# Performance work log

Hardware: AMD Instinct MI355X
Metric: run time of the kernel (lower is better)

Reference implementation:

```python
import jax, jax.numpy as jnp
import numpy as np

EMB_DIM = 1024
NUM_HEADS = 16
HEAD_DIM = EMB_DIM // NUM_HEADS


def setup_inputs() -> dict:
    key = jax.random.key(0)
    ks = jax.random.split(key, 6)
    B, S, D = 2, 2048, EMB_DIM
    x = jax.random.normal(ks[0], (B, S, D), dtype=jnp.float32)
    # torch nn.Linear default init: U(-1/sqrt(in), 1/sqrt(in)); weights stored [out,in]
    lim = 1.0 / np.sqrt(D)
    Wq = jax.random.uniform(ks[1], (D, D), jnp.float32, -lim, lim)
    Wk = jax.random.uniform(ks[2], (D, D), jnp.float32, -lim, lim)
    Wv = jax.random.uniform(ks[3], (D, D), jnp.float32, -lim, lim)
    Wo = jax.random.uniform(ks[4], (D, D), jnp.float32, -lim, lim)
    q_scale = jnp.ones((1, 1, D), jnp.float32)
    k_scale = jnp.ones((1, 1, D), jnp.float32)
    v_scale = jnp.ones((1, 1, D), jnp.float32)
    o_scale = jnp.ones((1, 1, D), jnp.float32)
    return {"x": x, "Wq": Wq, "Wk": Wk, "Wv": Wv, "Wo": Wo,
            "q_scale": q_scale, "k_scale": k_scale,
            "v_scale": v_scale, "o_scale": o_scale}


def reference(x, Wq, Wk, Wv, Wo, q_scale, k_scale, v_scale, o_scale):
    B, S, D = x.shape
    H, Hd = NUM_HEADS, HEAD_DIM
    # linear (torch: x @ W^T) then per-channel scale
    Q = (x @ Wq.T) * q_scale
    K = (x @ Wk.T) * k_scale
    V = (x @ Wv.T) * v_scale
    # [B, H, S, Hd]
    Q = Q.reshape(B, S, H, Hd).transpose(0, 2, 1, 3)
    K = K.reshape(B, S, H, Hd).transpose(0, 2, 1, 3)
    V = V.reshape(B, S, H, Hd).transpose(0, 2, 1, 3)
    scores = jnp.einsum("bhqd,bhkd->bhqk", Q, K) / jnp.sqrt(
        jnp.asarray(Hd, jnp.float32))
    probs = jax.nn.softmax(scores, axis=-1)
    ctx = jnp.einsum("bhqk,bhkd->bhqd", probs, V)
    ctx = ctx.transpose(0, 2, 1, 3).reshape(B, S, D)
    return (ctx @ Wo.T) * o_scale
```

## Files before the change

kernel.cpp:

```cpp
#include <hip/hip_runtime.h>
#include <hip/hip_bf16.h>
#include <stdint.h>


typedef __bf16 bf16;
typedef __attribute__((ext_vector_type(8))) __bf16 bf16x8;
typedef __attribute__((ext_vector_type(4))) __bf16 bf16x4;
typedef __attribute__((ext_vector_type(4))) float f32x4;

#define DEVI __device__ __forceinline__

DEVI void gl_lds16(const void* g, void* l) {
  __builtin_amdgcn_global_load_lds(
      (const __attribute__((address_space(1))) void*)g,
      (__attribute__((address_space(3))) void*)l, 16, 0, 0);
}

DEVI bf16x8 load8(const bf16* p) { return *(const bf16x8*)p; }
DEVI bf16x8 load8(const float* p) {
  f32x4 a = *(const f32x4*)p;
  f32x4 b = *(const f32x4*)(p + 4);
  bf16x8 r;
  r[0] = (bf16)a[0]; r[1] = (bf16)a[1]; r[2] = (bf16)a[2]; r[3] = (bf16)a[3];
  r[4] = (bf16)b[0]; r[5] = (bf16)b[1]; r[6] = (bf16)b[2]; r[7] = (bf16)b[3];
  return r;
}

__global__ __launch_bounds__(256)
void cvt_kernel(const float* __restrict__ x,
                const float* __restrict__ w0, const float* __restrict__ w1,
                const float* __restrict__ w2, const float* __restrict__ w3,
                bf16* __restrict__ xb, bf16* __restrict__ wb) {
  const int y = blockIdx.y;
  const float* src;
  bf16* dst;
  if (y < 4) {
    src = (y == 0) ? w0 : (y == 1) ? w1 : (y == 2) ? w2 : w3;
    dst = wb + (size_t)y * 1048576;
  } else {
    src = x + (size_t)(y - 4) * 1048576;
    dst = xb + (size_t)(y - 4) * 1048576;
  }
  const int i = (blockIdx.x * 256 + threadIdx.x) * 8;
  *(bf16x8*)(dst + i) = load8(src + i);
}

template <typename XT, typename WT, int NTILE>
__global__ __launch_bounds__(256, 2)
void gemm_kernel(const XT* __restrict__ X,
                 const WT* __restrict__ W0, const WT* __restrict__ W1,
                 const WT* __restrict__ W2,
                 const float* __restrict__ s0, const float* __restrict__ s1,
                 const float* __restrict__ s2,
                 bf16* __restrict__ o0, bf16* __restrict__ o1,
                 bf16* __restrict__ o2, float* __restrict__ ofp, int three) {
  constexpr int NF = NTILE / 32;
  constexpr bool ASYNC_A = (sizeof(XT) == 2);
  constexpr bool ASYNC_B = (sizeof(WT) == 2);
  __shared__ bf16 As[128 * 32];
  __shared__ bf16 Bs[NTILE * 32];

  const int t = threadIdx.x;
  const int lane = t & 63;
  const int w = t >> 6;
  const int wm = w >> 1, wn = w & 1;
  const int m0 = blockIdx.x * 128;
  const int cl = lane & 15, quad = lane >> 4;

  const WT* Wp; const float* sp; bf16* op; int mode, n0; float emul = 1.f;
  if (three) {
    int which = blockIdx.y >> 3;
    n0 = (blockIdx.y & 7) * 128;
    if (which == 0)      { Wp = W0; sp = s0; op = o0; mode = 1; emul = 0.18033688f; }
    else if (which == 1) { Wp = W1; sp = s1; op = o1; mode = 1; }
    else                 { Wp = W2; sp = s2; op = o2; mode = 2; }
  } else {
    n0 = blockIdx.y * NTILE; Wp = W0; sp = s0; op = o0; mode = 0;
  }

  f32x4 zero = {0.f, 0.f, 0.f, 0.f};
  f32x4 acc[4][NF];
#pragma unroll
  for (int i = 0; i < 4; i++)
#pragma unroll
    for (int j = 0; j < NF; j++) acc[i][j] = zero;

  const int srow = t >> 2;
  const int gcol_sw = ((t & 3) ^ (srow & 3)) * 8;
  const int gcol = (t & 3) * 8;
  const int sphys = (((t & 3) ^ (srow & 3)) << 3);

  for (int k0 = 0; k0 < 1024; k0 += 32) {
    bf16x8 a0, a1, b0, b1;
    if constexpr (!ASYNC_A) {
      a0 = load8(&X[(uint64_t)(m0 + srow) * 1024 + k0 + gcol]);
      a1 = load8(&X[(uint64_t)(m0 + 64 + srow) * 1024 + k0 + gcol]);
    }
    if constexpr (!ASYNC_B) {
      b0 = load8(&Wp[(uint64_t)(n0 + srow) * 1024 + k0 + gcol]);
      if constexpr (NTILE == 128)
        b1 = load8(&Wp[(uint64_t)(n0 + 64 + srow) * 1024 + k0 + gcol]);
    }
    __syncthreads();
    if constexpr (ASYNC_A) {
      gl_lds16(X + (uint64_t)(m0 + srow) * 1024 + k0 + gcol_sw, (char*)As + t * 16);
      gl_lds16(X + (uint64_t)(m0 + 64 + srow) * 1024 + k0 + gcol_sw,
               (char*)As + 4096 + t * 16);
    } else {
      *(bf16x8*)&As[srow * 32 + sphys] = a0;
      *(bf16x8*)&As[(64 + srow) * 32 + sphys] = a1;
    }
    if constexpr (ASYNC_B) {
      gl_lds16(Wp + (uint64_t)(n0 + srow) * 1024 + k0 + gcol_sw, (char*)Bs + t * 16);
      if constexpr (NTILE == 128)
        gl_lds16(Wp + (uint64_t)(n0 + 64 + srow) * 1024 + k0 + gcol_sw,
                 (char*)Bs + 4096 + t * 16);
    } else {
      *(bf16x8*)&Bs[srow * 32 + sphys] = b0;
      if constexpr (NTILE == 128)
        *(bf16x8*)&Bs[(64 + srow) * 32 + sphys] = b1;
    }
    __syncthreads();

    bf16x8 af[4], bfr[NF];
#pragma unroll
    for (int mt = 0; mt < 4; mt++) {
      const int row = wm * 64 + mt * 16 + cl;
      af[mt] = *(const bf16x8*)&As[row * 32 + ((quad ^ (cl & 3)) << 3)];
    }
#pragma unroll
    for (int nt = 0; nt < NF; nt++) {
      const int row = wn * (NF * 16) + nt * 16 + cl;
      bfr[nt] = *(const bf16x8*)&Bs[row * 32 + ((quad ^ (cl & 3)) << 3)];
    }
#pragma unroll
    for (int mt = 0; mt < 4; mt++)
#pragma unroll
      for (int nt = 0; nt < NF; nt++)
        acc[mt][nt] = __builtin_amdgcn_mfma_f32_16x16x32_bf16(af[mt], bfr[nt],
                                                              acc[mt][nt], 0, 0, 0);
  }

#pragma unroll
  for (int nt = 0; nt < NF; nt++) {
    const int gn = n0 + wn * (NF * 16) + nt * 16 + cl;
    const float sc = sp[gn] * emul;
#pragma unroll
    for (int mt = 0; mt < 4; mt++) {
      const int gmb = m0 + wm * 64 + mt * 16 + quad * 4;
#pragma unroll
      for (int r = 0; r < 4; r++) {
        const int gm = gmb + r;
        const float v = acc[mt][nt][r] * sc;
        if (mode == 0) {
          ofp[(uint64_t)gm * 1024 + gn] = v;
        } else {
          const int b = gm >> 11, s = gm & 2047;
          const int h = gn >> 6, hd = gn & 63;
          uint64_t addr;
          if (mode == 1) addr = ((uint64_t)(b * 16 + h) * 2048 + s) * 64 + hd;
          else           addr = ((uint64_t)(b * 16 + h) * 64 + hd) * 2048 + s;
          op[addr] = (bf16)v;
        }
      }
    }
  }
}

__global__ __launch_bounds__(256, 2)
void attn_kernel(const bf16* __restrict__ Qw, const bf16* __restrict__ Kw,
                 const bf16* __restrict__ Vtw, bf16* __restrict__ Ctx) {
  __shared__ bf16 Ks[64 * 64];
  __shared__ bf16 Vs[64 * 64];
  __shared__ bf16 Ps[8 * 16 * 64];

  const int t = threadIdx.x, lane = t & 63, w = t >> 6;
  const int cl = lane & 15, quad = lane >> 4;

  const int id = blockIdx.x;
  const int xcd = id & 7, k = id >> 3;
  const int bh = xcd * 4 + (k >> 4);
  const int qt = k & 15;
  const int b = bh >> 4, h = bh & 15;
  const int q0 = qt * 128;

  const bf16* Qh = Qw + (uint64_t)bh * 2048 * 64;
  const bf16* Kh = Kw + (uint64_t)bh * 2048 * 64;
  const bf16* Vh = Vtw + (uint64_t)bh * 64 * 2048;

  bf16x8 qf[2][2];
#pragma unroll
  for (int mt = 0; mt < 2; mt++) {
    const int r = q0 + mt * 64 + w * 16 + cl;
    qf[mt][0] = *(const bf16x8*)&Qh[(uint64_t)r * 64 + quad * 8];
    qf[mt][1] = *(const bf16x8*)&Qh[(uint64_t)r * 64 + 32 + quad * 8];
  }

  f32x4 zero = {0.f, 0.f, 0.f, 0.f};
  f32x4 o_acc[2][4];
  float lsum[2] = {0.f, 0.f};
#pragma unroll
  for (int mt = 0; mt < 2; mt++)
#pragma unroll
    for (int i = 0; i < 4; i++) o_acc[mt][i] = zero;

  const int srow = t >> 3;
  const int gcol_sw = ((t & 7) ^ (srow & 7)) * 8;
  const int psw = (cl & 7) << 1;

  for (int k0 = 0; k0 < 2048; k0 += 64) {
    __syncthreads();
    gl_lds16(Kh + (uint64_t)(k0 + srow) * 64 + gcol_sw,        (char*)Ks + t * 16);
    gl_lds16(Kh + (uint64_t)(k0 + 32 + srow) * 64 + gcol_sw,   (char*)Ks + 4096 + t * 16);
    gl_lds16(Vh + (uint64_t)srow * 2048 + k0 + gcol_sw,        (char*)Vs + t * 16);
    gl_lds16(Vh + (uint64_t)(32 + srow) * 2048 + k0 + gcol_sw, (char*)Vs + 4096 + t * 16);
    __syncthreads();

#pragma unroll
    for (int nt = 0; nt < 4; nt++) {
      const int krow = nt * 16 + cl;
      bf16x8 kf0 = *(const bf16x8*)&Ks[krow * 64 + ((quad ^ (cl & 7)) << 3)];
      bf16x8 kf1 = *(const bf16x8*)&Ks[krow * 64 + (((quad + 4) ^ (cl & 7)) << 3)];
#pragma unroll
      for (int mt = 0; mt < 2; mt++) {
        f32x4 s = __builtin_amdgcn_mfma_f32_16x16x32_bf16(kf0, qf[mt][0], zero, 0, 0, 0);
        s = __builtin_amdgcn_mfma_f32_16x16x32_bf16(kf1, qf[mt][1], s, 0, 0, 0);
        bf16x4 pk;
        float ls = 0.f;
#pragma unroll
        for (int r = 0; r < 4; r++) {
          const float p = __builtin_amdgcn_exp2f(s[r]);
          ls += p;
          pk[r] = (bf16)p;
        }
        lsum[mt] += ls;
        bf16* Pm = Ps + (w * 2 + mt) * 1024;
        const int c = 4 * nt + quad;
        *(bf16x4*)&Pm[cl * 64 + ((c ^ psw) << 2)] = pk;
      }
    }

    bf16x8 pf[2][2];
#pragma unroll
    for (int mt = 0; mt < 2; mt++) {
      const bf16* Pm = Ps + (w * 2 + mt) * 1024;
#pragma unroll
      for (int hh = 0; hh < 2; hh++) {
        const int c0 = 8 * hh + 2 * quad;
        pf[mt][hh] = *(const bf16x8*)&Pm[cl * 64 + ((c0 ^ psw) << 2)];
      }
    }

#pragma unroll
    for (int nt = 0; nt < 4; nt++) {
      const int vrow = nt * 16 + cl;
      bf16x8 v0 = *(const bf16x8*)&Vs[vrow * 64 + ((quad ^ (cl & 7)) << 3)];
      bf16x8 v1 = *(const bf16x8*)&Vs[vrow * 64 + (((quad + 4) ^ (cl & 7)) << 3)];
#pragma unroll
      for (int mt = 0; mt < 2; mt++) {
        o_acc[mt][nt] = __builtin_amdgcn_mfma_f32_16x16x32_bf16(pf[mt][0], v0,
                                                                o_acc[mt][nt], 0, 0, 0);
        o_acc[mt][nt] = __builtin_amdgcn_mfma_f32_16x16x32_bf16(pf[mt][1], v1,
                                                                o_acc[mt][nt], 0, 0, 0);
      }
    }
  }

  float linv[2][4];
#pragma unroll
  for (int mt = 0; mt < 2; mt++) {
    float l = lsum[mt];
    l += __shfl_xor(l, 16);
    l += __shfl_xor(l, 32);
#pragma unroll
    for (int r = 0; r < 4; r++)
      linv[mt][r] = 1.0f / __shfl(l, quad * 4 + r);
  }
#pragma unroll
  for (int mt = 0; mt < 2; mt++)
#pragma unroll
    for (int nt = 0; nt < 4; nt++)
#pragma unroll
      for (int r = 0; r < 4; r++) {
        const int s = q0 + mt * 64 + w * 16 + quad * 4 + r;
        const int hd = nt * 16 + cl;
        Ctx[(uint64_t)(b * 2048 + s) * 1024 + h * 64 + hd] =
            (bf16)(o_acc[mt][nt][r] * linv[mt][r]);
      }
}

extern "C" void kernel_launch(void* const* d_in, const int* in_sizes, int n_in,
                              void* d_out, int out_size, void* d_ws, size_t ws_size,
                              hipStream_t stream) {
  const float* x  = (const float*)d_in[0];
  const float* Wq = (const float*)d_in[1];
  const float* Wk = (const float*)d_in[2];
  const float* Wv = (const float*)d_in[3];
  const float* Wo = (const float*)d_in[4];
  const float* qs = (const float*)d_in[5];
  const float* ks = (const float*)d_in[6];
  const float* vs = (const float*)d_in[7];
  const float* os = (const float*)d_in[8];
  float* out = (float*)d_out;

  const size_t M4 = 4194304, M1 = 1048576;

  if (ws_size >= (size_t)40 * 1024 * 1024) {
    bf16* xb = (bf16*)d_ws;
    bf16* wb = xb + M4;
    bf16* qw = wb + M4;
    bf16* kw = qw + M4;
    bf16* vw = kw + M4;
    bf16* cw = xb;

    cvt_kernel<<<dim3(512, 8), 256, 0, stream>>>(x, Wq, Wk, Wv, Wo, xb, wb);
    gemm_kernel<bf16, bf16, 128><<<dim3(32, 24), 256, 0, stream>>>(
        xb, wb, wb + M1, wb + 2 * M1, qs, ks, vs, qw, kw, vw, nullptr, 1);
    attn_kernel<<<512, 256, 0, stream>>>(qw, kw, vw, cw);
    gemm_kernel<bf16, bf16, 64><<<dim3(32, 16), 256, 0, stream>>>(
        cw, wb + 3 * M1, nullptr, nullptr, os, nullptr, nullptr,
        nullptr, nullptr, nullptr, out, 0);
  } else {
    bf16* qw = (bf16*)d_ws;
    bf16* kw = qw + M4;
    bf16* vw = kw + M4;
    bf16* cw = vw + M4;
    gemm_kernel<float, float, 128><<<dim3(32, 24), 256, 0, stream>>>(
        x, Wq, Wk, Wv, qs, ks, vs, qw, kw, vw, nullptr, 1);
    attn_kernel<<<512, 256, 0, stream>>>(qw, kw, vw, cw);
    gemm_kernel<bf16, float, 64><<<dim3(32, 16), 256, 0, stream>>>(
        cw, Wo, nullptr, nullptr, os, nullptr, nullptr,
        nullptr, nullptr, nullptr, out, 0);
  }
}
```

Before: 196.4 us.

## Double-buffer LDS tiles in GEMM and attention kernels to overlap loads

Both the projection GEMM (bf16 path) and the attention kernel now keep two shared-memory buffers. The next K-tile (or K/V tile) is issued with async global-to-LDS loads while the current buffer is consumed by MFMAs, with one barrier per iteration instead of two. The goal is to hide global-memory latency behind matrix math. The cost is double the LDS footprint, which may limit occupancy. There is also a risk that the compiler's waitcnt handling of global_load_lds serializes the loads anyway.

```diff
diff --git a/kernel.cpp b/kernel.cpp
--- a/kernel.cpp
+++ b/kernel.cpp
@@ -55,10 +55,9 @@
                  bf16* __restrict__ o0, bf16* __restrict__ o1,
                  bf16* __restrict__ o2, float* __restrict__ ofp, int three) {
   constexpr int NF = NTILE / 32;
-  constexpr bool ASYNC_A = (sizeof(XT) == 2);
-  constexpr bool ASYNC_B = (sizeof(WT) == 2);
-  __shared__ bf16 As[128 * 32];
-  __shared__ bf16 Bs[NTILE * 32];
+  constexpr bool ASYNC = (sizeof(XT) == 2) && (sizeof(WT) == 2);
+  __shared__ bf16 As[2][128 * 32];
+  __shared__ bf16 Bs[2][NTILE * 32];
 
   const int t = threadIdx.x;
   const int lane = t & 63;
@@ -90,56 +89,81 @@
   const int gcol = (t & 3) * 8;
   const int sphys = (((t & 3) ^ (srow & 3)) << 3);
 
-  for (int k0 = 0; k0 < 1024; k0 += 32) {
-    bf16x8 a0, a1, b0, b1;
-    if constexpr (!ASYNC_A) {
-      a0 = load8(&X[(uint64_t)(m0 + srow) * 1024 + k0 + gcol]);
-      a1 = load8(&X[(uint64_t)(m0 + 64 + srow) * 1024 + k0 + gcol]);
-    }
-    if constexpr (!ASYNC_B) {
-      b0 = load8(&Wp[(uint64_t)(n0 + srow) * 1024 + k0 + gcol]);
-      if constexpr (NTILE == 128)
+#define STAGEG(bi, k0_)                                                        \
+  {                                                                            \
+    gl_lds16(X + (uint64_t)(m0 + srow) * 1024 + (k0_) + gcol_sw,               \
+             (char*)As[bi] + t * 16);                                          \
+    gl_lds16(X + (uint64_t)(m0 + 64 + srow) * 1024 + (k0_) + gcol_sw,          \
+             (char*)As[bi] + 4096 + t * 16);                                   \
+    gl_lds16(Wp + (uint64_t)(n0 + srow) * 1024 + (k0_) + gcol_sw,              \
+             (char*)Bs[bi] + t * 16);                                          \
+    if (NTILE == 128)                                                          \
+      gl_lds16(Wp + (uint64_t)(n0 + 64 + srow) * 1024 + (k0_) + gcol_sw,       \
+               (char*)Bs[bi] + 4096 + t * 16);                                 \
+  }
+
+  if constexpr (ASYNC) {
+    STAGEG(0, 0)
+    for (int it = 0; it < 32; it++) {
+      __syncthreads();
+      if (it < 31) STAGEG((it + 1) & 1, (it + 1) * 32)
+      const bf16* Ab = As[it & 1];
+      const bf16* Bb = Bs[it & 1];
+
+      bf16x8 af[4], bfr[NF];
+#pragma unroll
+      for (int mt = 0; mt < 4; mt++) {
+        const int row = wm * 64 + mt * 16 + cl;
+        af[mt] = *(const bf16x8*)&Ab[row * 32 + ((quad ^ (cl & 3)) << 3)];
+      }
+#pragma unroll
+      for (int nt = 0; nt < NF; nt++) {
+        const int row = wn * (NF * 16) + nt * 16 + cl;
+        bfr[nt] = *(const bf16x8*)&Bb[row * 32 + ((quad ^ (cl & 3)) << 3)];
+      }
+#pragma unroll
+      for (int mt = 0; mt < 4; mt++)
+#pragma unroll
+        for (int nt = 0; nt < NF; nt++)
+          acc[mt][nt] = __builtin_amdgcn_mfma_f32_16x16x32_bf16(
+              af[mt], bfr[nt], acc[mt][nt], 0, 0, 0);
+    }
+  } else {
+    for (int k0 = 0; k0 < 1024; k0 += 32) {
+      bf16x8 a0 = load8(&X[(uint64_t)(m0 + srow) * 1024 + k0 + gcol]);
+      bf16x8 a1 = load8(&X[(uint64_t)(m0 + 64 + srow) * 1024 + k0 + gcol]);
+      bf16x8 b0 = load8(&Wp[(uint64_t)(n0 + srow) * 1024 + k0 + gcol]);
+      bf16x8 b1;
+      if (NTILE == 128)
         b1 = load8(&Wp[(uint64_t)(n0 + 64 + srow) * 1024 + k0 + gcol]);
-    }
-    __syncthreads();
-    if constexpr (ASYNC_A) {
-      gl_lds16(X + (uint64_t)(m0 + srow) * 1024 + k0 + gcol_sw, (char*)As + t * 16);
-      gl_lds16(X + (uint64_t)(m0 + 64 + srow) * 1024 + k0 + gcol_sw,
-               (char*)As + 4096 + t * 16);
-    } else {
-      *(bf16x8*)&As[srow * 32 + sphys] = a0;
-      *(bf16x8*)&As[(64 + srow) * 32 + sphys] = a1;
-    }
-    if constexpr (ASYNC_B) {
-      gl_lds16(Wp + (uint64_t)(n0 + srow) * 1024 + k0 + gcol_sw, (char*)Bs + t * 16);
-      if constexpr (NTILE == 128)
-        gl_lds16(Wp + (uint64_t)(n0 + 64 + srow) * 1024 + k0 + gcol_sw,
-                 (char*)Bs + 4096 + t * 16);
-    } else {
-      *(bf16x8*)&Bs[srow * 32 + sphys] = b0;
-      if constexpr (NTILE == 128)
-        *(bf16x8*)&Bs[(64 + srow) * 32 + sphys] = b1;
-    }
-    __syncthreads();
-
-    bf16x8 af[4], bfr[NF];
-#pragma unroll
-    for (int mt = 0; mt < 4; mt++) {
-      const int row = wm * 64 + mt * 16 + cl;
-      af[mt] = *(const bf16x8*)&As[row * 32 + ((quad ^ (cl & 3)) << 3)];
-    }
-#pragma unroll
-    for (int nt = 0; nt < NF; nt++) {
-      const int row = wn * (NF * 16) + nt * 16 + cl;
-      bfr[nt] = *(const bf16x8*)&Bs[row * 32 + ((quad ^ (cl & 3)) << 3)];
-    }
-#pragma unroll
-    for (int mt = 0; mt < 4; mt++)
-#pragma unroll
-      for (int nt = 0; nt < NF; nt++)
-        acc[mt][nt] = __builtin_amdgcn_mfma_f32_16x16x32_bf16(af[mt], bfr[nt],
-                                                              acc[mt][nt], 0, 0, 0);
-  }
+      __syncthreads();
+      *(bf16x8*)&As[0][srow * 32 + sphys] = a0;
+      *(bf16x8*)&As[0][(64 + srow) * 32 + sphys] = a1;
+      *(bf16x8*)&Bs[0][srow * 32 + sphys] = b0;
+      if (NTILE == 128)
+        *(bf16x8*)&Bs[0][(64 + srow) * 32 + sphys] = b1;
+      __syncthreads();
+
+      bf16x8 af[4], bfr[NF];
+#pragma unroll
+      for (int mt = 0; mt < 4; mt++) {
+        const int row = wm * 64 + mt * 16 + cl;
+        af[mt] = *(const bf16x8*)&As[0][row * 32 + ((quad ^ (cl & 3)) << 3)];
+      }
+#pragma unroll
+      for (int nt = 0; nt < NF; nt++) {
+        const int row = wn * (NF * 16) + nt * 16 + cl;
+        bfr[nt] = *(const bf16x8*)&Bs[0][row * 32 + ((quad ^ (cl & 3)) << 3)];
+      }
+#pragma unroll
+      for (int mt = 0; mt < 4; mt++)
+#pragma unroll
+        for (int nt = 0; nt < NF; nt++)
+          acc[mt][nt] = __builtin_amdgcn_mfma_f32_16x16x32_bf16(
+              af[mt], bfr[nt], acc[mt][nt], 0, 0, 0);
+    }
+  }
+#undef STAGEG
 
 #pragma unroll
   for (int nt = 0; nt < NF; nt++) {
@@ -170,8 +194,8 @@
 __global__ __launch_bounds__(256, 2)
 void attn_kernel(const bf16* __restrict__ Qw, const bf16* __restrict__ Kw,
                  const bf16* __restrict__ Vtw, bf16* __restrict__ Ctx) {
-  __shared__ bf16 Ks[64 * 64];
-  __shared__ bf16 Vs[64 * 64];
+  __shared__ bf16 Ks[2][64 * 64];
+  __shared__ bf16 Vs[2][64 * 64];
   __shared__ bf16 Ps[8 * 16 * 64];
 
   const int t = threadIdx.x, lane = t & 63, w = t >> 6;
@@ -208,19 +232,31 @@
   const int gcol_sw = ((t & 7) ^ (srow & 7)) * 8;
   const int psw = (cl & 7) << 1;
 
-  for (int k0 = 0; k0 < 2048; k0 += 64) {
+#define STAGEA(bi, k0_)                                                        \
+  {                                                                            \
+    gl_lds16(Kh + (uint64_t)((k0_) + srow) * 64 + gcol_sw,                     \
+             (char*)Ks[bi] + t * 16);                                          \
+    gl_lds16(Kh + (uint64_t)((k0_) + 32 + srow) * 64 + gcol_sw,                \
+             (char*)Ks[bi] + 4096 + t * 16);                                   \
+    gl_lds16(Vh + (uint64_t)srow * 2048 + (k0_) + gcol_sw,                     \
+             (char*)Vs[bi] + t * 16);                                          \
+    gl_lds16(Vh + (uint64_t)(32 + srow) * 2048 + (k0_) + gcol_sw,              \
+             (char*)Vs[bi] + 4096 + t * 16);                                   \
+  }
+
+  STAGEA(0, 0)
+
+  for (int it = 0; it < 32; it++) {
     __syncthreads();
-    gl_lds16(Kh + (uint64_t)(k0 + srow) * 64 + gcol_sw,        (char*)Ks + t * 16);
-    gl_lds16(Kh + (uint64_t)(k0 + 32 + srow) * 64 + gcol_sw,   (char*)Ks + 4096 + t * 16);
-    gl_lds16(Vh + (uint64_t)srow * 2048 + k0 + gcol_sw,        (char*)Vs + t * 16);
-    gl_lds16(Vh + (uint64_t)(32 + srow) * 2048 + k0 + gcol_sw, (char*)Vs + 4096 + t * 16);
-    __syncthreads();
+    if (it < 31) STAGEA((it + 1) & 1, (it + 1) * 64)
+    const bf16* Ksb = Ks[it & 1];
+    const bf16* Vsb = Vs[it & 1];
 
 #pragma unroll
     for (int nt = 0; nt < 4; nt++) {
       const int krow = nt * 16 + cl;
-      bf16x8 kf0 = *(const bf16x8*)&Ks[krow * 64 + ((quad ^ (cl & 7)) << 3)];
-      bf16x8 kf1 = *(const bf16x8*)&Ks[krow * 64 + (((quad + 4) ^ (cl & 7)) << 3)];
+      bf16x8 kf0 = *(const bf16x8*)&Ksb[krow * 64 + ((quad ^ (cl & 7)) << 3)];
+      bf16x8 kf1 = *(const bf16x8*)&Ksb[krow * 64 + (((quad + 4) ^ (cl & 7)) << 3)];
 #pragma unroll
       for (int mt = 0; mt < 2; mt++) {
         f32x4 s = __builtin_amdgcn_mfma_f32_16x16x32_bf16(kf0, qf[mt][0], zero, 0, 0, 0);
@@ -254,8 +290,8 @@
 #pragma unroll
     for (int nt = 0; nt < 4; nt++) {
       const int vrow = nt * 16 + cl;
-      bf16x8 v0 = *(const bf16x8*)&Vs[vrow * 64 + ((quad ^ (cl & 7)) << 3)];
-      bf16x8 v1 = *(const bf16x8*)&Vs[vrow * 64 + (((quad + 4) ^ (cl & 7)) << 3)];
+      bf16x8 v0 = *(const bf16x8*)&Vsb[vrow * 64 + ((quad ^ (cl & 7)) << 3)];
+      bf16x8 v1 = *(const bf16x8*)&Vsb[vrow * 64 + (((quad + 4) ^ (cl & 7)) << 3)];
 #pragma unroll
       for (int mt = 0; mt < 2; mt++) {
         o_acc[mt][nt] = __builtin_amdgcn_mfma_f32_16x16x32_bf16(pf[mt][0], v0,
@@ -265,6 +301,7 @@
       }
     }
   }
+#undef STAGEA
 
   float linv[2][4];
 #pragma unroll
```

After: 202.3 us. +3.0%, slower.

## Split attention KV tile across wave pairs with LDS reduction of partial outputs

Applied to the files above, without the earlier changes.

Reorganizes the attention kernel so each pair of waves shares a 64-query block and splits the 64-key tile in halves, with each wave handling 4 query subtiles. K and V fragments are loaded once per wave into registers and reused across 4 query tiles, which cuts LDS reads per MFMA. Partial row sums and output accumulators are combined through new LDS buffers at the end. In exchange it doubles accumulator registers, which may hurt occupancy under launch_bounds(256,2), and adds a final LDS reduction pass.

```diff
diff --git a/kernel.cpp b/kernel.cpp
--- a/kernel.cpp
+++ b/kernel.cpp
@@ -172,15 +172,18 @@
                  const bf16* __restrict__ Vtw, bf16* __restrict__ Ctx) {
   __shared__ bf16 Ks[64 * 64];
   __shared__ bf16 Vs[64 * 64];
-  __shared__ bf16 Ps[8 * 16 * 64];
+  __shared__ bf16 Ps[4][64 * 32];
+  __shared__ float Lbuf[4 * 64];
+  __shared__ float Obuf[2][4096];
 
   const int t = threadIdx.x, lane = t & 63, w = t >> 6;
   const int cl = lane & 15, quad = lane >> 4;
+  const int wq = w >> 1, wk = w & 1;
 
   const int id = blockIdx.x;
-  const int xcd = id & 7, k = id >> 3;
-  const int bh = xcd * 4 + (k >> 4);
-  const int qt = k & 15;
+  const int xcd = id & 7, kk = id >> 3;
+  const int bh = xcd * 4 + (kk >> 4);
+  const int qt = kk & 15;
   const int b = bh >> 4, h = bh & 15;
   const int q0 = qt * 128;
 
@@ -188,25 +191,25 @@
   const bf16* Kh = Kw + (uint64_t)bh * 2048 * 64;
   const bf16* Vh = Vtw + (uint64_t)bh * 64 * 2048;
 
-  bf16x8 qf[2][2];
-#pragma unroll
-  for (int mt = 0; mt < 2; mt++) {
-    const int r = q0 + mt * 64 + w * 16 + cl;
+  bf16x8 qf[4][2];
+#pragma unroll
+  for (int mt = 0; mt < 4; mt++) {
+    const int r = q0 + wq * 64 + mt * 16 + cl;
     qf[mt][0] = *(const bf16x8*)&Qh[(uint64_t)r * 64 + quad * 8];
     qf[mt][1] = *(const bf16x8*)&Qh[(uint64_t)r * 64 + 32 + quad * 8];
   }
 
   f32x4 zero = {0.f, 0.f, 0.f, 0.f};
-  f32x4 o_acc[2][4];
-  float lsum[2] = {0.f, 0.f};
-#pragma unroll
-  for (int mt = 0; mt < 2; mt++)
-#pragma unroll
-    for (int i = 0; i < 4; i++) o_acc[mt][i] = zero;
+  f32x4 o_acc[4][4];
+  float lsum[4] = {0.f, 0.f, 0.f, 0.f};
+#pragma unroll
+  for (int mt = 0; mt < 4; mt++)
+#pragma unroll
+    for (int nt = 0; nt < 4; nt++) o_acc[mt][nt] = zero;
 
   const int srow = t >> 3;
   const int gcol_sw = ((t & 7) ^ (srow & 7)) * 8;
-  const int psw = (cl & 7) << 1;
+  bf16* Pw = Ps[w];
 
   for (int k0 = 0; k0 < 2048; k0 += 64) {
     __syncthreads();
@@ -216,15 +219,28 @@
     gl_lds16(Vh + (uint64_t)(32 + srow) * 2048 + k0 + gcol_sw, (char*)Vs + 4096 + t * 16);
     __syncthreads();
 
-#pragma unroll
-    for (int nt = 0; nt < 4; nt++) {
-      const int krow = nt * 16 + cl;
-      bf16x8 kf0 = *(const bf16x8*)&Ks[krow * 64 + ((quad ^ (cl & 7)) << 3)];
-      bf16x8 kf1 = *(const bf16x8*)&Ks[krow * 64 + (((quad + 4) ^ (cl & 7)) << 3)];
-#pragma unroll
-      for (int mt = 0; mt < 2; mt++) {
-        f32x4 s = __builtin_amdgcn_mfma_f32_16x16x32_bf16(kf0, qf[mt][0], zero, 0, 0, 0);
-        s = __builtin_amdgcn_mfma_f32_16x16x32_bf16(kf1, qf[mt][1], s, 0, 0, 0);
+    bf16x8 kf[2][2];
+#pragma unroll
+    for (int knt = 0; knt < 2; knt++) {
+      const int krow = wk * 32 + knt * 16 + cl;
+#pragma unroll
+      for (int hh = 0; hh < 2; hh++)
+        kf[knt][hh] = *(const bf16x8*)&Ks[krow * 64 +
+                                          (((hh * 4 + quad) ^ (cl & 7)) << 3)];
+    }
+    bf16x8 vf[4];
+#pragma unroll
+    for (int nt = 0; nt < 4; nt++)
+      vf[nt] = *(const bf16x8*)&Vs[(nt * 16 + cl) * 64 +
+                                   (((wk * 4 + quad) ^ (cl & 7)) << 3)];
+
+#pragma unroll
+    for (int mt = 0; mt < 4; mt++) {
+#pragma unroll
+      for (int knt = 0; knt < 2; knt++) {
+        f32x4 s = __builtin_amdgcn_mfma_f32_16x16x32_bf16(kf[knt][0], qf[mt][0],
+                                                          zero, 0, 0, 0);
+        s = __builtin_amdgcn_mfma_f32_16x16x32_bf16(kf[knt][1], qf[mt][1], s, 0, 0, 0);
         bf16x4 pk;
         float ls = 0.f;
 #pragma unroll
@@ -234,59 +250,61 @@
           pk[r] = (bf16)p;
         }
         lsum[mt] += ls;
-        bf16* Pm = Ps + (w * 2 + mt) * 1024;
-        const int c = 4 * nt + quad;
-        *(bf16x4*)&Pm[cl * 64 + ((c ^ psw) << 2)] = pk;
+        const int row = mt * 16 + cl;
+        const int u = knt * 4 + quad;
+        *(bf16x4*)&Pw[row * 32 + ((u ^ (cl & 6)) << 2)] = pk;
       }
     }
 
-    bf16x8 pf[2][2];
-#pragma unroll
-    for (int mt = 0; mt < 2; mt++) {
-      const bf16* Pm = Ps + (w * 2 + mt) * 1024;
-#pragma unroll
-      for (int hh = 0; hh < 2; hh++) {
-        const int c0 = 8 * hh + 2 * quad;
-        pf[mt][hh] = *(const bf16x8*)&Pm[cl * 64 + ((c0 ^ psw) << 2)];
-      }
-    }
-
-#pragma unroll
-    for (int nt = 0; nt < 4; nt++) {
-      const int vrow = nt * 16 + cl;
-      bf16x8 v0 = *(const bf16x8*)&Vs[vrow * 64 + ((quad ^ (cl & 7)) << 3)];
-      bf16x8 v1 = *(const bf16x8*)&Vs[vrow * 64 + (((quad + 4) ^ (cl & 7)) << 3)];
-#pragma unroll
-      for (int mt = 0; mt < 2; mt++) {
-        o_acc[mt][nt] = __builtin_amdgcn_mfma_f32_16x16x32_bf16(pf[mt][0], v0,
+#pragma unroll
+    for (int mt = 0; mt < 4; mt++) {
+      const int row = mt * 16 + cl;
+      bf16x8 pf = *(const bf16x8*)&Pw[row * 32 + (((2 * quad) ^ (cl & 6)) << 2)];
+#pragma unroll
+      for (int nt = 0; nt < 4; nt++)
+        o_acc[mt][nt] = __builtin_amdgcn_mfma_f32_16x16x32_bf16(pf, vf[nt],
                                                                 o_acc[mt][nt], 0, 0, 0);
-        o_acc[mt][nt] = __builtin_amdgcn_mfma_f32_16x16x32_bf16(pf[mt][1], v1,
-                                                                o_acc[mt][nt], 0, 0, 0);
-      }
-    }
-  }
-
-  float linv[2][4];
-#pragma unroll
-  for (int mt = 0; mt < 2; mt++) {
+    }
+  }
+
+#pragma unroll
+  for (int mt = 0; mt < 4; mt++) {
     float l = lsum[mt];
     l += __shfl_xor(l, 16);
     l += __shfl_xor(l, 32);
-#pragma unroll
-    for (int r = 0; r < 4; r++)
-      linv[mt][r] = 1.0f / __shfl(l, quad * 4 + r);
-  }
-#pragma unroll
-  for (int mt = 0; mt < 2; mt++)
-#pragma unroll
-    for (int nt = 0; nt < 4; nt++)
+    if (lane < 16) Lbuf[w * 64 + mt * 16 + lane] = l;
+  }
+  __syncthreads();
+  if (wk == 1) {
+#pragma unroll
+    for (int mt = 0; mt < 4; mt++)
+#pragma unroll
+      for (int nt = 0; nt < 4; nt++)
+        *(f32x4*)&Obuf[wq][(mt * 4 + nt) * 256 + lane * 4] = o_acc[mt][nt];
+  }
+  __syncthreads();
+  if (wk == 0) {
+#pragma unroll
+    for (int mt = 0; mt < 4; mt++) {
+      float linv[4];
 #pragma unroll
       for (int r = 0; r < 4; r++) {
-        const int s = q0 + mt * 64 + w * 16 + quad * 4 + r;
-        const int hd = nt * 16 + cl;
-        Ctx[(uint64_t)(b * 2048 + s) * 1024 + h * 64 + hd] =
-            (bf16)(o_acc[mt][nt][r] * linv[mt][r]);
+        const int ql = mt * 16 + quad * 4 + r;
+        linv[r] = 1.0f / (Lbuf[(wq * 2) * 64 + ql] + Lbuf[(wq * 2 + 1) * 64 + ql]);
       }
+#pragma unroll
+      for (int nt = 0; nt < 4; nt++) {
+        f32x4 other = *(const f32x4*)&Obuf[wq][(mt * 4 + nt) * 256 + lane * 4];
+#pragma unroll
+        for (int r = 0; r < 4; r++) {
+          const int q = q0 + wq * 64 + mt * 16 + quad * 4 + r;
+          const int hd = nt * 16 + cl;
+          Ctx[(uint64_t)(b * 2048 + q) * 1024 + h * 64 + hd] =
+              (bf16)((o_acc[mt][nt][r] + other[r]) * linv[r]);
+        }
+      }
+    }
+  }
 }
 
 extern "C" void kernel_launch(void* const* d_in, const int* in_sizes, int n_in,
```

New measurement: 190.5 us. -3.0%, faster.
